# Performance work log

Hardware: AMD Instinct MI355X
Metric: run time of the kernel (lower is better)

Reference implementation:

```python
import jax, jax.numpy as jnp
import numpy as np

MARGIN = 1.0  # init kwarg 'margin'
NUM_CLASSES = 16


def setup_inputs() -> dict:
    key = jax.random.key(0)
    k1, k2 = jax.random.split(key)
    embeddings = jax.random.normal(k1, (384, 1024), dtype=jnp.float32)
    labels = jax.random.randint(k2, (384,), 0, NUM_CLASSES, dtype=jnp.int64)
    return {"embeddings": embeddings, "labels": labels}


def reference(embeddings, labels):
    # Dense, on-device equivalent of the CPU triplet mining:
    # valid triplet (a, p, n) iff labels[a]==labels[p], a<p, labels[n]!=labels[a].
    # Mean over all valid triplets == original torch losses.mean().
    B = embeddings.shape[0]
    sq = jnp.sum(embeddings * embeddings, axis=1)                      # [B]
    # Squared pairwise distances via Gram matrix (same math as (x_i-x_j)^2.sum())
    D = sq[:, None] + sq[None, :] - 2.0 * (embeddings @ embeddings.T)  # [B,B]

    eq = labels[:, None] == labels[None, :]                            # same-label mask [B,B]
    idx = jnp.arange(B)
    ap_valid = eq & (idx[:, None] < idx[None, :])                      # anchor<positive pairs
    mask = ap_valid[:, :, None] & (~eq)[:, None, :]                    # [a,p,n] valid triplets

    # loss[a,p,n] = relu(D[a,p] - D[a,n] + margin)
    loss = jax.nn.relu(D[:, :, None] - D[:, None, :] + MARGIN)         # [B,B,B]

    count = jnp.sum(mask)
    total = jnp.sum(jnp.where(mask, loss, jnp.float32(0.0)))
    mean = jnp.where(count > 0, total / count.astype(loss.dtype), jnp.float32(0.0))
    return mean, count
```

## Files before the change

kernel.cpp:

```cpp
#include <hip/hip_runtime.h>


constexpr int BN  = 384;
constexpr int DIM = 1024;
constexpr float MARGIN = 1.0f;

__global__ __launch_bounds__(256) void gram_kernel(
    const float* __restrict__ E, float* __restrict__ P,
    float* __restrict__ sqpart, float* __restrict__ total,
    int* __restrict__ cnt, int KC) {
    __shared__ float Ast[32 * 34];
    __shared__ float Bst[32 * 34];
    const int tx = threadIdx.x, ty = threadIdx.y;
    const int t  = ty * 16 + tx;
    const int i0 = blockIdx.y * 32, j0 = blockIdx.x * 32;
    const int z  = blockIdx.z;
    const int lrow = t >> 3;
    const int lc4  = (t & 7) * 4;

    if (z == 0 && blockIdx.x == 0 && blockIdx.y == 0 && t == 0) {
        *total = 0.f; *cnt = 0;
    }

    const float* Arow = E + (size_t)(i0 + lrow) * DIM + z * KC + lc4;
    const float* Brow = E + (size_t)(j0 + lrow) * DIM + z * KC + lc4;

    float4 av = *reinterpret_cast<const float4*>(Arow);
    float4 bv = *reinterpret_cast<const float4*>(Brow);

    float acc00 = 0.f, acc01 = 0.f, acc10 = 0.f, acc11 = 0.f;

    for (int kt = 0; kt < KC; kt += 32) {
        Ast[(lc4 + 0) * 34 + lrow] = av.x; Ast[(lc4 + 1) * 34 + lrow] = av.y;
        Ast[(lc4 + 2) * 34 + lrow] = av.z; Ast[(lc4 + 3) * 34 + lrow] = av.w;
        Bst[(lc4 + 0) * 34 + lrow] = bv.x; Bst[(lc4 + 1) * 34 + lrow] = bv.y;
        Bst[(lc4 + 2) * 34 + lrow] = bv.z; Bst[(lc4 + 3) * 34 + lrow] = bv.w;
        __syncthreads();
        if (kt + 32 < KC) {
            av = *reinterpret_cast<const float4*>(Arow + kt + 32);
            bv = *reinterpret_cast<const float4*>(Brow + kt + 32);
        }
#pragma unroll
        for (int kk = 0; kk < 32; ++kk) {
            const float2 a01 = *reinterpret_cast<const float2*>(&Ast[kk * 34 + 2 * ty]);
            const float2 b01 = *reinterpret_cast<const float2*>(&Bst[kk * 34 + 2 * tx]);
            acc00 += a01.x * b01.x; acc01 += a01.x * b01.y;
            acc10 += a01.y * b01.x; acc11 += a01.y * b01.y;
        }
        __syncthreads();
    }

    const int r0 = i0 + 2 * ty;
    const int c0 = j0 + 2 * tx;
    float* Pz = P + (size_t)z * BN * BN;
    Pz[(size_t)r0 * BN + c0]           = acc00;
    Pz[(size_t)r0 * BN + c0 + 1]       = acc01;
    Pz[(size_t)(r0 + 1) * BN + c0]     = acc10;
    Pz[(size_t)(r0 + 1) * BN + c0 + 1] = acc11;
    if (blockIdx.x == blockIdx.y && tx == ty) {
        sqpart[z * BN + r0]     = acc00;
        sqpart[z * BN + r0 + 1] = acc11;
    }
}

__global__ __launch_bounds__(256) void triplet_kernel(
    const float* __restrict__ P, const float* __restrict__ sqpart,
    const int* __restrict__ labels, float* __restrict__ total,
    int* __restrict__ cnt, int NZ) {
    __shared__ float Hrow[BN];
    __shared__ int   lab[BN];
    __shared__ int   poslist[BN];
    __shared__ int   npos_s;
    __shared__ float wsum[4];
    __shared__ int   wcnt[4];
    const int a   = blockIdx.x;
    const int tid = threadIdx.x;

    if (tid == 0) npos_s = 0;
    for (int i = tid; i < BN; i += 256) {
        float g = 0.f, s = 0.f;
        for (int zz = 0; zz < NZ; ++zz) {
            g += P[(size_t)zz * BN * BN + (size_t)a * BN + i];
            s += sqpart[zz * BN + i];
        }
        Hrow[i] = s - 2.f * g;
        lab[i]  = labels[i];
    }
    __syncthreads();
    const int la = lab[a];

    int lc = 0;
    for (int p = tid; p < BN; p += 256) {
        if (lab[p] != la) ++lc;
        else if (p > a) { int k = atomicAdd(&npos_s, 1); poslist[k] = p; }
    }
    __syncthreads();
    const int np = npos_s;

    const float hn0  = Hrow[tid];
    const bool  neg0 = (lab[tid] != la);
    const bool  has1 = (tid + 256 < BN);
    const float hn1  = has1 ? Hrow[tid + 256] : 0.f;
    const bool  neg1 = has1 && (lab[tid + 256] != la);

    float ls = 0.f;
    for (int k = 0; k < np; ++k) {
        const float dpm = Hrow[poslist[k]] + MARGIN;
        if (neg0) { const float v = dpm - hn0; ls += (v > 0.f) ? v : 0.f; }
        if (neg1) { const float v = dpm - hn1; ls += (v > 0.f) ? v : 0.f; }
    }

#pragma unroll
    for (int off = 32; off; off >>= 1) {
        ls += __shfl_down(ls, off);
        lc += __shfl_down(lc, off);
    }
    const int wave = tid >> 6, lane = tid & 63;
    if (lane == 0) { wsum[wave] = ls; wcnt[wave] = lc; }
    __syncthreads();
    if (tid == 0) {
        const float s    = wsum[0] + wsum[1] + wsum[2] + wsum[3];
        const int   nneg = wcnt[0] + wcnt[1] + wcnt[2] + wcnt[3];
        if (s != 0.f) atomicAdd(total, s);
        if (np)       atomicAdd(cnt, np * nneg);
    }
}

__global__ void finalize_kernel(const float* __restrict__ total,
                                const int* __restrict__ cnt,
                                float* __restrict__ out) {
    if (threadIdx.x == 0) {
        const int c = *cnt;
        out[0] = (c > 0) ? (*total) / (float)c : 0.f;
        out[1] = (float)c;
    }
}

extern "C" void kernel_launch(void* const* d_in, const int* in_sizes, int n_in,
                              void* d_out, int out_size, void* d_ws, size_t ws_size,
                              hipStream_t stream) {
    const float* E      = (const float*)d_in[0];
    const int*   labels = (const int*)d_in[1];
    float*       out    = (float*)d_out;

    int Z = 1;
    for (int cand : {8, 4, 2}) {
        size_t need = (size_t)cand * BN * BN * 4 + (size_t)cand * BN * 4 + 64;
        if (need <= ws_size) { Z = cand; break; }
    }

    char*  ws     = (char*)d_ws;
    float* P      = (float*)ws;
    float* sqpart = (float*)(ws + (size_t)Z * BN * BN * 4);
    float* total  = (float*)(ws + (size_t)Z * BN * BN * 4 + (size_t)Z * BN * 4);
    int*   cnt    = (int*)(total + 1);

    gram_kernel<<<dim3(BN / 32, BN / 32, Z), dim3(16, 16), 0, stream>>>(
        E, P, sqpart, total, cnt, DIM / Z);
    triplet_kernel<<<BN, 256, 0, stream>>>(P, sqpart, labels, total, cnt, Z);
    finalize_kernel<<<1, 64, 0, stream>>>(total, cnt, out);
}
```

Before: 83.94 us.

## Use 64x64 Gram tiles with 4x4 microtiles, fuse finalize, shrink triplet blocks

The Gram kernel now computes 64x64 output tiles, with each thread holding a 4x4 accumulator, and uses float4 shared-memory reads with an XOR swizzle. This raises arithmetic intensity per shared load. Split-K can now go up to 16 partitions, and the partial-product layout is interleaved per row so the triplet kernel can read it with vectorized loads. The triplet kernel is templated on the partition count and runs 128 threads per block. The separate finalize launch is replaced by a last-block ticket pattern, which saves one launch but adds a threadfence and an extra atomic.

Measured after the change: 82.33 us. No clear change (-1.9%).

```diff
diff --git a/kernel.cpp b/kernel.cpp
--- a/kernel.cpp
+++ b/kernel.cpp
@@ -4,110 +4,142 @@
 constexpr int BN  = 384;
 constexpr int DIM = 1024;
 constexpr float MARGIN = 1.0f;
+constexpr int LDK = 68;
 
 __global__ __launch_bounds__(256) void gram_kernel(
     const float* __restrict__ E, float* __restrict__ P,
     float* __restrict__ sqpart, float* __restrict__ total,
-    int* __restrict__ cnt, int KC) {
-    __shared__ float Ast[32 * 34];
-    __shared__ float Bst[32 * 34];
+    int* __restrict__ cnt, int* __restrict__ ticket, int KC, int NZ) {
+    __shared__ float Ast[32 * LDK];
+    __shared__ float Bst[32 * LDK];
     const int tx = threadIdx.x, ty = threadIdx.y;
     const int t  = ty * 16 + tx;
-    const int i0 = blockIdx.y * 32, j0 = blockIdx.x * 32;
+    const int i0 = blockIdx.y * 64, j0 = blockIdx.x * 64;
     const int z  = blockIdx.z;
-    const int lrow = t >> 3;
-    const int lc4  = (t & 7) * 4;
 
     if (z == 0 && blockIdx.x == 0 && blockIdx.y == 0 && t == 0) {
-        *total = 0.f; *cnt = 0;
+        *total = 0.f; *cnt = 0; *ticket = 0;
     }
 
-    const float* Arow = E + (size_t)(i0 + lrow) * DIM + z * KC + lc4;
-    const float* Brow = E + (size_t)(j0 + lrow) * DIM + z * KC + lc4;
+    const int r  = t >> 2;
+    const int kq = t & 3;
+    const int kb = kq * 8;
+    const int rs = r ^ (kq << 4);
 
-    float4 av = *reinterpret_cast<const float4*>(Arow);
-    float4 bv = *reinterpret_cast<const float4*>(Brow);
+    const float* Ab = E + (size_t)(i0 + r) * DIM + z * KC + kb;
+    const float* Bb = E + (size_t)(j0 + r) * DIM + z * KC + kb;
 
-    float acc00 = 0.f, acc01 = 0.f, acc10 = 0.f, acc11 = 0.f;
+    float4 a0 = *(const float4*)(Ab);
+    float4 a1 = *(const float4*)(Ab + 4);
+    float4 b0 = *(const float4*)(Bb);
+    float4 b1 = *(const float4*)(Bb + 4);
+
+    float acc[4][4] = {};
 
     for (int kt = 0; kt < KC; kt += 32) {
-        Ast[(lc4 + 0) * 34 + lrow] = av.x; Ast[(lc4 + 1) * 34 + lrow] = av.y;
-        Ast[(lc4 + 2) * 34 + lrow] = av.z; Ast[(lc4 + 3) * 34 + lrow] = av.w;
-        Bst[(lc4 + 0) * 34 + lrow] = bv.x; Bst[(lc4 + 1) * 34 + lrow] = bv.y;
-        Bst[(lc4 + 2) * 34 + lrow] = bv.z; Bst[(lc4 + 3) * 34 + lrow] = bv.w;
+        Ast[(kb + 0) * LDK + rs] = a0.x; Ast[(kb + 1) * LDK + rs] = a0.y;
+        Ast[(kb + 2) * LDK + rs] = a0.z; Ast[(kb + 3) * LDK + rs] = a0.w;
+        Ast[(kb + 4) * LDK + rs] = a1.x; Ast[(kb + 5) * LDK + rs] = a1.y;
+        Ast[(kb + 6) * LDK + rs] = a1.z; Ast[(kb + 7) * LDK + rs] = a1.w;
+        Bst[(kb + 0) * LDK + rs] = b0.x; Bst[(kb + 1) * LDK + rs] = b0.y;
+        Bst[(kb + 2) * LDK + rs] = b0.z; Bst[(kb + 3) * LDK + rs] = b0.w;
+        Bst[(kb + 4) * LDK + rs] = b1.x; Bst[(kb + 5) * LDK + rs] = b1.y;
+        Bst[(kb + 6) * LDK + rs] = b1.z; Bst[(kb + 7) * LDK + rs] = b1.w;
         __syncthreads();
         if (kt + 32 < KC) {
-            av = *reinterpret_cast<const float4*>(Arow + kt + 32);
-            bv = *reinterpret_cast<const float4*>(Brow + kt + 32);
+            a0 = *(const float4*)(Ab + kt + 32);
+            a1 = *(const float4*)(Ab + kt + 36);
+            b0 = *(const float4*)(Bb + kt + 32);
+            b1 = *(const float4*)(Bb + kt + 36);
         }
 #pragma unroll
         for (int kk = 0; kk < 32; ++kk) {
-            const float2 a01 = *reinterpret_cast<const float2*>(&Ast[kk * 34 + 2 * ty]);
-            const float2 b01 = *reinterpret_cast<const float2*>(&Bst[kk * 34 + 2 * tx]);
-            acc00 += a01.x * b01.x; acc01 += a01.x * b01.y;
-            acc10 += a01.y * b01.x; acc11 += a01.y * b01.y;
+            const int sw = (kk >> 3) << 4;
+            const float4 av = *(const float4*)&Ast[kk * LDK + ((4 * ty) ^ sw)];
+            const float4 bv = *(const float4*)&Bst[kk * LDK + ((4 * tx) ^ sw)];
+            const float aa[4] = {av.x, av.y, av.z, av.w};
+            const float bb[4] = {bv.x, bv.y, bv.z, bv.w};
+#pragma unroll
+            for (int i2 = 0; i2 < 4; ++i2)
+#pragma unroll
+                for (int j2 = 0; j2 < 4; ++j2)
+                    acc[i2][j2] += aa[i2] * bb[j2];
         }
         __syncthreads();
     }
 
-    const int r0 = i0 + 2 * ty;
-    const int c0 = j0 + 2 * tx;
-    float* Pz = P + (size_t)z * BN * BN;
-    Pz[(size_t)r0 * BN + c0]           = acc00;
-    Pz[(size_t)r0 * BN + c0 + 1]       = acc01;
-    Pz[(size_t)(r0 + 1) * BN + c0]     = acc10;
-    Pz[(size_t)(r0 + 1) * BN + c0 + 1] = acc11;
+    const size_t rowstride = (size_t)NZ * BN;
+#pragma unroll
+    for (int i2 = 0; i2 < 4; ++i2) {
+        const float4 w = make_float4(acc[i2][0], acc[i2][1], acc[i2][2], acc[i2][3]);
+        *(float4*)&P[(size_t)(i0 + 4 * ty + i2) * rowstride + (size_t)z * BN + (j0 + 4 * tx)] = w;
+    }
     if (blockIdx.x == blockIdx.y && tx == ty) {
-        sqpart[z * BN + r0]     = acc00;
-        sqpart[z * BN + r0 + 1] = acc11;
+#pragma unroll
+        for (int i2 = 0; i2 < 4; ++i2)
+            sqpart[z * BN + (i0 + 4 * ty + i2)] = acc[i2][i2];
     }
 }
 
-__global__ __launch_bounds__(256) void triplet_kernel(
+template <int NZ>
+__global__ __launch_bounds__(128) void triplet_kernel(
     const float* __restrict__ P, const float* __restrict__ sqpart,
     const int* __restrict__ labels, float* __restrict__ total,
-    int* __restrict__ cnt, int NZ) {
+    int* __restrict__ cnt, int* __restrict__ ticket, float* __restrict__ out) {
     __shared__ float Hrow[BN];
     __shared__ int   lab[BN];
     __shared__ int   poslist[BN];
     __shared__ int   npos_s;
-    __shared__ float wsum[4];
-    __shared__ int   wcnt[4];
+    __shared__ float wsum[2];
+    __shared__ int   wcnt[2];
     const int a   = blockIdx.x;
     const int tid = threadIdx.x;
 
     if (tid == 0) npos_s = 0;
-    for (int i = tid; i < BN; i += 256) {
-        float g = 0.f, s = 0.f;
-        for (int zz = 0; zz < NZ; ++zz) {
-            g += P[(size_t)zz * BN * BN + (size_t)a * BN + i];
-            s += sqpart[zz * BN + i];
+    for (int i = tid; i < BN; i += 128) lab[i] = labels[i];
+
+    if (tid < 96) {
+        const int c0 = tid * 4;
+        float4 g = make_float4(0.f, 0.f, 0.f, 0.f);
+        float4 s = make_float4(0.f, 0.f, 0.f, 0.f);
+#pragma unroll
+        for (int z = 0; z < NZ; ++z) {
+            const float4 pv = *(const float4*)&P[(size_t)a * ((size_t)NZ * BN) + z * BN + c0];
+            const float4 sv = *(const float4*)&sqpart[z * BN + c0];
+            g.x += pv.x; g.y += pv.y; g.z += pv.z; g.w += pv.w;
+            s.x += sv.x; s.y += sv.y; s.z += sv.z; s.w += sv.w;
         }
-        Hrow[i] = s - 2.f * g;
-        lab[i]  = labels[i];
+        Hrow[c0 + 0] = s.x - 2.f * g.x;
+        Hrow[c0 + 1] = s.y - 2.f * g.y;
+        Hrow[c0 + 2] = s.z - 2.f * g.z;
+        Hrow[c0 + 3] = s.w - 2.f * g.w;
     }
     __syncthreads();
+
     const int la = lab[a];
-
     int lc = 0;
-    for (int p = tid; p < BN; p += 256) {
+#pragma unroll
+    for (int q = 0; q < 3; ++q) {
+        const int p = tid + q * 128;
         if (lab[p] != la) ++lc;
-        else if (p > a) { int k = atomicAdd(&npos_s, 1); poslist[k] = p; }
+        else if (p > a) { const int k = atomicAdd(&npos_s, 1); poslist[k] = p; }
     }
     __syncthreads();
     const int np = npos_s;
 
-    const float hn0  = Hrow[tid];
-    const bool  neg0 = (lab[tid] != la);
-    const bool  has1 = (tid + 256 < BN);
-    const float hn1  = has1 ? Hrow[tid + 256] : 0.f;
-    const bool  neg1 = has1 && (lab[tid + 256] != la);
+    const float hn0 = Hrow[tid];
+    const float hn1 = Hrow[tid + 128];
+    const float hn2 = Hrow[tid + 256];
+    const bool  ng0 = (lab[tid]       != la);
+    const bool  ng1 = (lab[tid + 128] != la);
+    const bool  ng2 = (lab[tid + 256] != la);
 
     float ls = 0.f;
     for (int k = 0; k < np; ++k) {
         const float dpm = Hrow[poslist[k]] + MARGIN;
-        if (neg0) { const float v = dpm - hn0; ls += (v > 0.f) ? v : 0.f; }
-        if (neg1) { const float v = dpm - hn1; ls += (v > 0.f) ? v : 0.f; }
+        if (ng0) { const float v = dpm - hn0; ls += (v > 0.f) ? v : 0.f; }
+        if (ng1) { const float v = dpm - hn1; ls += (v > 0.f) ? v : 0.f; }
+        if (ng2) { const float v = dpm - hn2; ls += (v > 0.f) ? v : 0.f; }
     }
 
 #pragma unroll
@@ -119,20 +151,18 @@
     if (lane == 0) { wsum[wave] = ls; wcnt[wave] = lc; }
     __syncthreads();
     if (tid == 0) {
-        const float s    = wsum[0] + wsum[1] + wsum[2] + wsum[3];
-        const int   nneg = wcnt[0] + wcnt[1] + wcnt[2] + wcnt[3];
+        const float s    = wsum[0] + wsum[1];
+        const int   nneg = wcnt[0] + wcnt[1];
         if (s != 0.f) atomicAdd(total, s);
         if (np)       atomicAdd(cnt, np * nneg);
-    }
-}
-
-__global__ void finalize_kernel(const float* __restrict__ total,
-                                const int* __restrict__ cnt,
-                                float* __restrict__ out) {
-    if (threadIdx.x == 0) {
-        const int c = *cnt;
-        out[0] = (c > 0) ? (*total) / (float)c : 0.f;
-        out[1] = (float)c;
+        __threadfence();
+        const int done = atomicAdd(ticket, 1);
+        if (done == (int)gridDim.x - 1) {
+            const float tot = atomicAdd(total, 0.0f);
+            const int   c   = atomicAdd(cnt, 0);
+            out[0] = (c > 0) ? tot / (float)c : 0.f;
+            out[1] = (float)c;
+        }
     }
 }
 
@@ -144,7 +174,7 @@
     float*       out    = (float*)d_out;
 
     int Z = 1;
-    for (int cand : {8, 4, 2}) {
+    for (int cand : {16, 8, 4, 2}) {
         size_t need = (size_t)cand * BN * BN * 4 + (size_t)cand * BN * 4 + 64;
         if (need <= ws_size) { Z = cand; break; }
     }
@@ -154,9 +184,16 @@
     float* sqpart = (float*)(ws + (size_t)Z * BN * BN * 4);
     float* total  = (float*)(ws + (size_t)Z * BN * BN * 4 + (size_t)Z * BN * 4);
     int*   cnt    = (int*)(total + 1);
+    int*   ticket = (int*)(total + 2);
 
-    gram_kernel<<<dim3(BN / 32, BN / 32, Z), dim3(16, 16), 0, stream>>>(
-        E, P, sqpart, total, cnt, DIM / Z);
-    triplet_kernel<<<BN, 256, 0, stream>>>(P, sqpart, labels, total, cnt, Z);
-    finalize_kernel<<<1, 64, 0, stream>>>(total, cnt, out);
+    gram_kernel<<<dim3(6, 6, Z), dim3(16, 16), 0, stream>>>(
+        E, P, sqpart, total, cnt, ticket, DIM / Z, Z);
+
+    switch (Z) {
+        case 16: triplet_kernel<16><<<BN, 128, 0, stream>>>(P, sqpart, labels, total, cnt, ticket, out); break;
+        case 8:  triplet_kernel<8> <<<BN, 128, 0, stream>>>(P, sqpart, labels, total, cnt, ticket, out); break;
+        case 4:  triplet_kernel<4> <<<BN, 128, 0, stream>>>(P, sqpart, labels, total, cnt, ticket, out); break;
+        case 2:  triplet_kernel<2> <<<BN, 128, 0, stream>>>(P, sqpart, labels, total, cnt, ticket, out); break;
+        default: triplet_kernel<1> <<<BN, 128, 0, stream>>>(P, sqpart, labels, total, cnt, ticket, out); break;
+    }
 }
```
